# Kernel tuning notes

Measured on AMD Instinct MI355X. Metric: run time of the kernel, lower is better.

## Reference

```python
import jax, jax.numpy as jnp
import numpy as np

B, BINS, EMBED, HID, IND = 1, 500, 1024, 512, 128
POOL, MC_CROP, HIC_CROP = 5, 50, 10


def setup_inputs() -> dict:
    key = jax.random.key(0)
    ks = jax.random.split(key, 10)
    def w(k, shape, fan_in):
        return (jax.random.normal(k, shape, jnp.float32) / np.sqrt(fan_in)).astype(jnp.float32)
    return dict(
        x=jax.random.normal(ks[0], (B, BINS, EMBED), jnp.float32),
        # project MLP
        p_w1=w(ks[1], (EMBED, HID), EMBED), p_b1=jnp.zeros((HID,), jnp.float32),
        p_w2=w(ks[2], (HID, HID), HID), p_b2=jnp.zeros((HID,), jnp.float32),
        # pairattn_cop stub: per-pair linears (micro at full res, hic after 5x5 avg-pool)
        micro_w=w(ks[3], (HID, IND), HID), micro_b=jnp.zeros((IND,), jnp.float32),
        hic_w=w(ks[4], (HID, IND), HID), hic_b=jnp.zeros((IND,), jnp.float32),
        # prediction heads
        head_mc_w=w(ks[5], (IND, 2), IND), head_mc_b=jnp.zeros((2,), jnp.float32),
        head_ih_w1=w(ks[6], (IND, IND // 2), IND), head_ih_b1=jnp.zeros((IND // 2,), jnp.float32),
        head_ih_w2=w(ks[7], (IND // 2, 2), IND // 2), head_ih_b2=jnp.zeros((2,), jnp.float32),
        head_hic_w=w(ks[8], (IND, 3), IND), head_hic_b=jnp.zeros((3,), jnp.float32),
    )


def reference(x, p_w1, p_b1, p_w2, p_b2, micro_w, micro_b, hic_w, hic_b,
              head_mc_w, head_mc_b, head_ih_w1, head_ih_b1, head_ih_w2, head_ih_b2,
              head_hic_w, head_hic_b):
    # project: Linear -> ReLU -> Linear
    h = jax.nn.relu(x @ p_w1 + p_b1) @ p_w2 + p_b2            # [B, bins, HID]
    # output_head: fused pairwise outer-sum mean + scaled elementwise dot
    xi = h[:, :, None, :]                                      # [B, bins, 1, HID]
    xj = h[:, None, :, :]                                      # [B, 1, bins, HID]
    pair = (xi + xj) * 0.5 + xi * xj * (1.0 / np.sqrt(HID))    # [B, bins, bins, HID]
    # pairattn_cop stub
    micro = pair @ micro_w + micro_b                           # [B, bins, bins, IND]
    nb = BINS // POOL
    hic_in = pair.reshape(B, nb, POOL, nb, POOL, HID).mean(axis=(2, 4))  # [B, nb, nb, HID]
    hic = hic_in @ hic_w + hic_b                               # [B, nb, nb, IND]
    # prediction heads with crops
    mc = micro[:, MC_CROP:-MC_CROP, MC_CROP:-MC_CROP, :]       # [B, 400, 400, IND]
    out_mc = mc @ head_mc_w + head_mc_b
    out_ih = jax.nn.relu(mc @ head_ih_w1 + head_ih_b1) @ head_ih_w2 + head_ih_b2
    hc = hic[:, HIC_CROP:-HIC_CROP, HIC_CROP:-HIC_CROP, :]     # [B, 80, 80, IND]
    out_hic = hc @ head_hic_w + head_hic_b
    return (out_mc, out_ih, micro, out_hic)
```

## Files before the change

### kernel.cpp

```cpp
#include <hip/hip_runtime.h>

#define BINS 500
#define HID  512
#define INDD 128
#define PAIR_S 0.044194173824159216f

#define OFF_MC    0
#define OFF_IH    320000
#define OFF_MICRO 640000
#define OFF_HIC   32640000

#define WS_U     0
#define WS_MWT   64000
#define WS_HBF   96768
#define WS_H     256000
#define WS_HBAR  512000
#define WS_HWT   563200
#define WS_W1CT  595968

typedef __bf16 bf16;
typedef bf16 bf16x4 __attribute__((ext_vector_type(4)));
typedef bf16 bf16x8 __attribute__((ext_vector_type(8)));
typedef float f32x4 __attribute__((ext_vector_type(4)));

__device__ __forceinline__ bf16x8 join8(bf16x4 lo, bf16x4 hi) {
  return __builtin_shufflevector(lo, hi, 0, 1, 2, 3, 4, 5, 6, 7);
}
__device__ __forceinline__ bf16x4 cvt4(float a, float b, float c, float d) {
  bf16x4 r; r[0] = (bf16)a; r[1] = (bf16)b; r[2] = (bf16)c; r[3] = (bf16)d; return r;
}

__global__ void zero_init(float* __restrict__ ws) {
  int idx = (blockIdx.x * 256 + threadIdx.x) * 4;
  float4 z = {0.f, 0.f, 0.f, 0.f};
  *(float4*)(ws + idx) = z;
  *(float4*)(ws + WS_H + idx) = z;
}

__global__ __launch_bounds__(256, 2)
void gemm_ks(const float* __restrict__ A, const float* __restrict__ B,
             const float* __restrict__ abias, float* __restrict__ C,
             int M, int N, int K_per, int a_relu, float scale) {
  __shared__ float a_lds[64][36];
  __shared__ float bt_lds[64][36];
  const int t = threadIdx.x;
  const int w = t >> 6, l = t & 63;
  const int lr = l & 15, g = l >> 4;
  const int r0 = blockIdx.x * 64, n0 = blockIdx.y * 64;
  const int kbase = blockIdx.z * K_per;
  f32x4 acc[4] = {};
  for (int kq = 0; kq < K_per; kq += 32) {
    const int k0 = kbase + kq;
    {
      int row = t >> 2, kc = (t & 3) * 8;
      int gr = r0 + row; gr = gr < M ? gr : M - 1;
      const float* src = A + (size_t)gr * K_per * gridDim.z + k0 + kc;
      float4 v0 = *(const float4*)src;
      float4 v1 = *(const float4*)(src + 4);
      if (abias) {
        const float* bp = abias + k0 + kc;
        v0.x += bp[0]; v0.y += bp[1]; v0.z += bp[2]; v0.w += bp[3];
        v1.x += bp[4]; v1.y += bp[5]; v1.z += bp[6]; v1.w += bp[7];
        if (a_relu) {
          v0.x = fmaxf(v0.x, 0.f); v0.y = fmaxf(v0.y, 0.f);
          v0.z = fmaxf(v0.z, 0.f); v0.w = fmaxf(v0.w, 0.f);
          v1.x = fmaxf(v1.x, 0.f); v1.y = fmaxf(v1.y, 0.f);
          v1.z = fmaxf(v1.z, 0.f); v1.w = fmaxf(v1.w, 0.f);
        }
      }
      *(float4*)&a_lds[row][kc]     = v0;
      *(float4*)&a_lds[row][kc + 4] = v1;
    }
    {
      int n = t & 63, ks = (t >> 6) * 8;
      const float* src = B + (size_t)(k0 + ks) * N + n0 + n;
      #pragma unroll
      for (int s = 0; s < 8; s++) bt_lds[n][ks + s] = src[(size_t)s * N];
    }
    __syncthreads();
    bf16x8 ahi, alo;
    {
      int row = w * 16 + lr;
      float4 u0 = *(const float4*)&a_lds[row][g * 8];
      float4 u1 = *(const float4*)&a_lds[row][g * 8 + 4];
      float v[8] = {u0.x, u0.y, u0.z, u0.w, u1.x, u1.y, u1.z, u1.w};
      #pragma unroll
      for (int e = 0; e < 8; e++) {
        bf16 h = (bf16)v[e];
        ahi[e] = h; alo[e] = (bf16)(v[e] - (float)h);
      }
    }
    #pragma unroll
    for (int fn = 0; fn < 4; fn++) {
      int col = fn * 16 + lr;
      float4 u0 = *(const float4*)&bt_lds[col][g * 8];
      float4 u1 = *(const float4*)&bt_lds[col][g * 8 + 4];
      float v[8] = {u0.x, u0.y, u0.z, u0.w, u1.x, u1.y, u1.z, u1.w};
      bf16x8 bhi, blo;
      #pragma unroll
      for (int e = 0; e < 8; e++) {
        bf16 h = (bf16)v[e];
        bhi[e] = h; blo[e] = (bf16)(v[e] - (float)h);
      }
      acc[fn] = __builtin_amdgcn_mfma_f32_16x16x32_bf16(ahi, bhi, acc[fn], 0, 0, 0);
      acc[fn] = __builtin_amdgcn_mfma_f32_16x16x32_bf16(ahi, blo, acc[fn], 0, 0, 0);
      acc[fn] = __builtin_amdgcn_mfma_f32_16x16x32_bf16(alo, bhi, acc[fn], 0, 0, 0);
    }
    __syncthreads();
  }
  #pragma unroll
  for (int fn = 0; fn < 4; fn++) {
    int col = n0 + fn * 16 + lr;
    #pragma unroll
    for (int r = 0; r < 4; r++) {
      int row = r0 + w * 16 + g * 4 + r;
      if (row < M) atomicAdd(&C[(size_t)row * N + col], acc[fn][r] * scale);
    }
  }
}

__global__ void post_h(const float* __restrict__ h, const float* __restrict__ b2,
                       const float* __restrict__ micro_w,
                       const float* __restrict__ hic_w, const float* __restrict__ w_ih1,
                       const float* __restrict__ w_mc, float* __restrict__ ws) {
  int g = blockIdx.x * 256 + threadIdx.x;
  if (g < 256000) {
    bf16* hbf = (bf16*)(ws + WS_HBF);
    int k = g & (HID - 1);
    hbf[g] = (bf16)(h[g] + b2[k]);
  } else if (g < 256000 + 65536) {
    int gg = g - 256000;
    int n = gg >> 9, k = gg & 511;
    bf16* mwt = (bf16*)(ws + WS_MWT);
    mwt[gg] = (bf16)(PAIR_S * micro_w[k * INDD + n]);
  } else if (g < 256000 + 65536 + 51200) {
    int gg = g - (256000 + 65536);
    int a = gg >> 9, k = gg & (HID - 1);
    const float* p = h + (size_t)(a * 5) * HID + k;
    ws[WS_HBAR + gg] = 0.2f * (p[0] + p[HID] + p[2 * HID] + p[3 * HID] + p[4 * HID]) + b2[k];
  } else if (g < 256000 + 65536 + 51200 + 65536) {
    int gg = g - (256000 + 65536 + 51200);
    int n = gg >> 9, k = gg & 511;
    bf16* hwt = (bf16*)(ws + WS_HWT);
    hwt[gg] = (bf16)hic_w[k * INDD + n];
  } else if (g < 256000 + 65536 + 51200 + 65536 + 10240) {
    int gg = g - (256000 + 65536 + 51200 + 65536);
    int n = gg >> 7, k = gg & 127;
    float v = 0.f;
    if (n < 64) v = w_ih1[k * 64 + n];
    else if (n < 66) v = w_mc[k * 2 + (n - 64)];
    bf16* w1c = (bf16*)(ws + WS_W1CT);
    w1c[gg] = (bf16)v;
  } else if (g < 256000 + 65536 + 51200 + 65536 + 10240 + 64000) {
    int gg = g - (256000 + 65536 + 51200 + 65536 + 10240);
    ws[WS_U + gg] = 0.f;
  }
}

__global__ __launch_bounds__(256, 3)
void fused_micro_heads(const float* __restrict__ wsf, const float* __restrict__ micro_b,
                       const float* __restrict__ b1, const float* __restrict__ w2,
                       const float* __restrict__ bmc, const float* __restrict__ b2,
                       float* __restrict__ out) {
  __shared__ bf16 smem[16384];
  const int t = threadIdx.x;
  const int wv = t >> 6, l = t & 63;
  const int wj = wv >> 1, wn = wv & 1;
  const int lr = l & 15, g = l >> 4;
  const int i  = blockIdx.x;
  const int j0 = blockIdx.y * 128;
  const bf16* Hbf = (const bf16*)(wsf + WS_HBF);
  const bf16* mwt = (const bf16*)(wsf + WS_MWT);
  const float* U  = wsf + WS_U;
  const int bn = t >> 1, bh = t & 1;
  const int arow   = l >> 2;
  const int achunk = (l & 3) ^ ((l >> 3) & 3);
  const bf16* hbi = Hbf + (size_t)i * HID;
  f32x4 acc[4][4] = {};

  #pragma unroll
  for (int q = 0; q < 2; q++) {
    int row = wv * 32 + q * 16 + arow;
    int jj = j0 + row; jj = jj < BINS ? jj : BINS - 1;
    __builtin_amdgcn_global_load_lds(
        (const __attribute__((address_space(1))) void*)(Hbf + (size_t)jj * HID + achunk * 8),
        (__attribute__((address_space(3))) void*)(smem + (wv * 32 + q * 16) * 32),
        16, 0, 0);
  }
  {
    bf16x8 w0 = *(const bf16x8*)(mwt + (size_t)bn * HID + bh * 16);
    bf16x8 w1 = *(const bf16x8*)(mwt + (size_t)bn * HID + bh * 16 + 8);
    bf16x8 h0 = *(const bf16x8*)(hbi + bh * 16);
    bf16x8 h1 = *(const bf16x8*)(hbi + bh * 16 + 8);
    bf16x8 o0, o1;
    #pragma unroll
    for (int e = 0; e < 8; e++) o0[e] = (bf16)((float)h0[e] * (float)w0[e]);
    #pragma unroll
    for (int e = 0; e < 8; e++) o1[e] = (bf16)((float)h1[e] * (float)w1[e]);
    const int sw = (bn >> 1) & 3;
    *(bf16x8*)(smem + 8192 + bn * 32 + ((bh * 2)     ^ sw) * 8) = o0;
    *(bf16x8*)(smem + 8192 + bn * 32 + ((bh * 2 + 1) ^ sw) * 8) = o1;
  }
  asm volatile("s_waitcnt vmcnt(0) lgkmcnt(0)" ::: "memory");
  __builtin_amdgcn_s_barrier();

  int cur = 0;
  for (int kt = 0; kt < 16; kt++) {
    const bf16* htc = smem + cur * 4096;
    const bf16* btc = smem + 8192 + cur * 4096;
    bf16x8 w0, w1, h0, h1;
    if (kt < 15) {
      const int kn = (kt + 1) * 32;
      w0 = *(const bf16x8*)(mwt + (size_t)bn * HID + kn + bh * 16);
      w1 = *(const bf16x8*)(mwt + (size_t)bn * HID + kn + bh * 16 + 8);
      h0 = *(const bf16x8*)(hbi + kn + bh * 16);
      h1 = *(const bf16x8*)(hbi + kn + bh * 16 + 8);
      #pragma unroll
      for (int q = 0; q < 2; q++) {
        int row = wv * 32 + q * 16 + arow;
        int jj = j0 + row; jj = jj < BINS ? jj : BINS - 1;
        __builtin_amdgcn_global_load_lds(
            (const __attribute__((address_space(1))) void*)(Hbf + (size_t)jj * HID + kn + achunk * 8),
            (__attribute__((address_space(3))) void*)(smem + (cur ^ 1) * 4096 + (wv * 32 + q * 16) * 32),
            16, 0, 0);
      }
      asm volatile("s_waitcnt vmcnt(6)" ::: "memory");
    } else {
      asm volatile("s_waitcnt vmcnt(0)" ::: "memory");
    }
    bf16x8 af[4], bfr[4];
    const int s = g ^ ((lr >> 1) & 3);
    #pragma unroll
    for (int fm = 0; fm < 4; fm++)
      af[fm] = *(const bf16x8*)(htc + (wj * 64 + fm * 16 + lr) * 32 + s * 8);
    #pragma unroll
    for (int fn = 0; fn < 4; fn++)
      bfr[fn] = *(const bf16x8*)(btc + (wn * 64 + fn * 16 + lr) * 32 + s * 8);
    #pragma unroll
    for (int fm = 0; fm < 4; fm++)
      #pragma unroll
      for (int fn = 0; fn < 4; fn++)
        acc[fm][fn] = __builtin_amdgcn_mfma_f32_16x16x32_bf16(af[fm], bfr[fn], acc[fm][fn], 0, 0, 0);
    if (kt < 15) {
      bf16x8 o0, o1;
      #pragma unroll
      for (int e = 0; e < 8; e++) o0[e] = (bf16)((float)h0[e] * (float)w0[e]);
      #pragma unroll
      for (int e = 0; e < 8; e++) o1[e] = (bf16)((float)h1[e] * (float)w1[e]);
      bf16* btn = smem + 8192 + (cur ^ 1) * 4096;
      const int sw = (bn >> 1) & 3;
      *(bf16x8*)(btn + bn * 32 + ((bh * 2)     ^ sw) * 8) = o0;
      *(bf16x8*)(btn + bn * 32 + ((bh * 2 + 1) ^ sw) * 8) = o1;
    }
    asm volatile("s_waitcnt lgkmcnt(0)" ::: "memory");
    __builtin_amdgcn_s_barrier();
    cur ^= 1;
  }

  float Ui[4];
  #pragma unroll
  for (int fn = 0; fn < 4; fn++) {
    int n = wn * 64 + fn * 16 + lr;
    Ui[fn] = U[(size_t)i * INDD + n] + micro_b[n];
  }
  #pragma unroll
  for (int fm = 0; fm < 4; fm++) {
    #pragma unroll
    for (int r = 0; r < 4; r++) {
      int j = j0 + wj * 64 + fm * 16 + g * 4 + r;
      if (j < BINS) {
        const float* Uj = U + (size_t)j * INDD;
        size_t base = (size_t)OFF_MICRO + ((size_t)i * BINS + j) * INDD;
        #pragma unroll
        for (int fn = 0; fn < 4; fn++) {
          int n = wn * 64 + fn * 16 + lr;
          out[base + n] = acc[fm][fn][r] + Ui[fn] + Uj[n];
        }
      }
    }
  }
  asm volatile("s_waitcnt vmcnt(0)" ::: "memory");
  __builtin_amdgcn_s_barrier();

  if (i >= 50 && i < 450) {
    const bf16* w1c = (const bf16*)(wsf + WS_W1CT);
    f32x4 acc2[2][5] = {};
    const int jg = wv * 32;
    #pragma unroll
    for (int kt2 = 0; kt2 < 4; kt2++) {
      const int k0 = kt2 * 32;
      bf16x8 bfr[5];
      #pragma unroll
      for (int fn = 0; fn < 5; fn++) {
        int q = fn * 16 + lr;
        bfr[fn] = *(const bf16x8*)(w1c + q * 128 + k0 + g * 8);
      }
      bf16x8 af2[2];
      #pragma unroll
      for (int s16 = 0; s16 < 2; s16++) {
        int j = j0 + jg + s16 * 16 + lr;
        int jc = j < BINS ? j : BINS - 1;
        const float* src = out + (size_t)OFF_MICRO + ((size_t)i * BINS + jc) * INDD + k0 + g * 8;
        float4 v0 = *(const float4*)src;
        float4 v1 = *(const float4*)(src + 4);
        af2[s16] = join8(cvt4(v0.x, v0.y, v0.z, v0.w), cvt4(v1.x, v1.y, v1.z, v1.w));
      }
      #pragma unroll
      for (int s16 = 0; s16 < 2; s16++)
        #pragma unroll
        for (int fn = 0; fn < 5; fn++)
          acc2[s16][fn] = __builtin_amdgcn_mfma_f32_16x16x32_bf16(af2[s16], bfr[fn], acc2[s16][fn], 0, 0, 0);
    }
    float w2a[4], w2b[4], b1v[4];
    #pragma unroll
    for (int fn = 0; fn < 4; fn++) {
      int q = fn * 16 + lr;
      w2a[fn] = w2[q * 2]; w2b[fn] = w2[q * 2 + 1]; b1v[fn] = b1[q];
    }
    float bm = (lr < 2) ? bmc[lr] : 0.f;
    float b2a = b2[0], b2bv = b2[1];
    #pragma unroll
    for (int s16 = 0; s16 < 2; s16++) {
      #pragma unroll
      for (int r = 0; r < 4; r++) {
        int j = j0 + jg + s16 * 16 + g * 4 + r;
        float s0 = 0.f, s1 = 0.f;
        #pragma unroll
        for (int fn = 0; fn < 4; fn++) {
          float v = fmaxf(acc2[s16][fn][r] + b1v[fn], 0.f);
          s0 += v * w2a[fn]; s1 += v * w2b[fn];
        }
        #pragma unroll
        for (int mk = 1; mk < 16; mk <<= 1) {
          s0 += __shfl_xor(s0, mk);
          s1 += __shfl_xor(s1, mk);
        }
        if (j >= 50 && j < 450) {
          size_t mo = (size_t)(i - 50) * 400 + (j - 50);
          if (lr == 0) {
            out[OFF_IH + mo * 2]     = s0 + b2a;
            out[OFF_IH + mo * 2 + 1] = s1 + b2bv;
          }
          if (lr < 2) out[OFF_MC + mo * 2 + lr] = acc2[s16][4][r] + bm;
        }
      }
    }
  }
}

__device__ __forceinline__ bf16x4 pair4(float4 a, float4 b) {
  bf16x4 r;
  r[0] = (bf16)((a.x + b.x) * 0.5f + a.x * b.x * PAIR_S);
  r[1] = (bf16)((a.y + b.y) * 0.5f + a.y * b.y * PAIR_S);
  r[2] = (bf16)((a.z + b.z) * 0.5f + a.z * b.z * PAIR_S);
  r[3] = (bf16)((a.w + b.w) * 0.5f + a.w * b.w * PAIR_S);
  return r;
}

__global__ __launch_bounds__(256, 2)
void hic_kernel(const float* __restrict__ hbar, const float* __restrict__ wsf,
                const float* __restrict__ hicb, const float* __restrict__ whic,
                const float* __restrict__ bhic, float* __restrict__ out) {
  __shared__ float ha_lds[16][36];
  __shared__ float hb_lds[16][36];
  __shared__ bf16 pair_lds[256][36];
  __shared__ bf16 bt_lds[128][36];
  const int t = threadIdx.x;
  const int wv = t >> 6, l = t & 63;
  const int lr = l & 15, g = l >> 4;
  const int a0 = 10 + blockIdx.x * 16, b0 = 10 + blockIdx.y * 16;
  const bf16* hwt = (const bf16*)(wsf + WS_HWT);
  f32x4 acc[4][8] = {};
  for (int kt = 0; kt < 16; kt++) {
    const int k0 = kt * 32;
    if (t < 64) {
      int row = t >> 2, c = (t & 3) * 8;
      const float* src = hbar + (size_t)(a0 + row) * HID + k0 + c;
      *(float4*)&ha_lds[row][c]     = *(const float4*)src;
      *(float4*)&ha_lds[row][c + 4] = *(const float4*)(src + 4);
    } else if (t < 128) {
      int tt = t - 64;
      int row = tt >> 2, c = (tt & 3) * 8;
      const float* src = hbar + (size_t)(b0 + row) * HID + k0 + c;
      *(float4*)&hb_lds[row][c]     = *(const float4*)src;
      *(float4*)&hb_lds[row][c + 4] = *(const float4*)(src + 4);
    } else {
      int tt = t - 128;
      #pragma unroll
      for (int rep = 0; rep < 4; rep++) {
        int chunk = tt * 4 + rep;
        int n = chunk >> 2, part = chunk & 3;
        bf16x8 v = *(const bf16x8*)(hwt + (size_t)n * HID + k0 + part * 8);
        *(bf16x4*)&bt_lds[n][part * 8]     = __builtin_shufflevector(v, v, 0, 1, 2, 3);
        *(bf16x4*)&bt_lds[n][part * 8 + 4] = __builtin_shufflevector(v, v, 4, 5, 6, 7);
      }
    }
    __syncthreads();
    {
      int m = t;
      const float* pa = &ha_lds[m >> 4][0];
      const float* pb = &hb_lds[m & 15][0];
      #pragma unroll
      for (int c = 0; c < 4; c++) {
        float4 av0 = *(const float4*)(pa + c * 8);
        float4 av1 = *(const float4*)(pa + c * 8 + 4);
        float4 bv0 = *(const float4*)(pb + c * 8);
        float4 bv1 = *(const float4*)(pb + c * 8 + 4);
        *(bf16x4*)&pair_lds[m][c * 8]     = pair4(av0, bv0);
        *(bf16x4*)&pair_lds[m][c * 8 + 4] = pair4(av1, bv1);
      }
    }
    __syncthreads();
    bf16x8 af[4], bfr[8];
    #pragma unroll
    for (int fm = 0; fm < 4; fm++) {
      int row = wv * 64 + fm * 16 + lr;
      af[fm] = join8(*(const bf16x4*)&pair_lds[row][g * 8],
                     *(const bf16x4*)&pair_lds[row][g * 8 + 4]);
    }
    #pragma unroll
    for (int fn = 0; fn < 8; fn++) {
      int col = fn * 16 + lr;
      bfr[fn] = join8(*(const bf16x4*)&bt_lds[col][g * 8],
                      *(const bf16x4*)&bt_lds[col][g * 8 + 4]);
    }
    #pragma unroll
    for (int fm = 0; fm < 4; fm++)
      #pragma unroll
      for (int fn = 0; fn < 8; fn++)
        acc[fm][fn] = __builtin_amdgcn_mfma_f32_16x16x32_bf16(af[fm], bfr[fn], acc[fm][fn], 0, 0, 0);
    __syncthreads();
  }
  float wh0[8], wh1[8], wh2[8], hbv[8];
  #pragma unroll
  for (int fn = 0; fn < 8; fn++) {
    int n = fn * 16 + lr;
    wh0[fn] = whic[n * 3]; wh1[fn] = whic[n * 3 + 1]; wh2[fn] = whic[n * 3 + 2];
    hbv[fn] = hicb[n];
  }
  float bh0 = bhic[0], bh1 = bhic[1], bh2 = bhic[2];
  #pragma unroll
  for (int fm = 0; fm < 4; fm++) {
    #pragma unroll
    for (int r = 0; r < 4; r++) {
      int m = wv * 64 + fm * 16 + g * 4 + r;
      float s0 = 0.f, s1 = 0.f, s2 = 0.f;
      #pragma unroll
      for (int fn = 0; fn < 8; fn++) {
        float v = acc[fm][fn][r] + hbv[fn];
        s0 += v * wh0[fn]; s1 += v * wh1[fn]; s2 += v * wh2[fn];
      }
      #pragma unroll
      for (int mk = 1; mk < 16; mk <<= 1) {
        s0 += __shfl_xor(s0, mk);
        s1 += __shfl_xor(s1, mk);
        s2 += __shfl_xor(s2, mk);
      }
      if (lr == 0) {
        int aa = a0 + (m >> 4) - 10, bb = b0 + (m & 15) - 10;
        size_t o = (size_t)OFF_HIC + (size_t)(aa * 80 + bb) * 3;
        out[o] = s0 + bh0; out[o + 1] = s1 + bh1; out[o + 2] = s2 + bh2;
      }
    }
  }
}

extern "C" void kernel_launch(void* const* d_in, const int* in_sizes, int n_in,
                              void* d_out, int out_size, void* d_ws, size_t ws_size,
                              hipStream_t stream) {
  (void)in_sizes; (void)n_in; (void)out_size; (void)ws_size;
  const float* x    = (const float*)d_in[0];
  const float* pw1  = (const float*)d_in[1];
  const float* pb1  = (const float*)d_in[2];
  const float* pw2  = (const float*)d_in[3];
  const float* pb2  = (const float*)d_in[4];
  const float* mw   = (const float*)d_in[5];
  const float* mb   = (const float*)d_in[6];
  const float* hw   = (const float*)d_in[7];
  const float* hb   = (const float*)d_in[8];
  const float* wmc  = (const float*)d_in[9];
  const float* bmc  = (const float*)d_in[10];
  const float* wih1 = (const float*)d_in[11];
  const float* bih1 = (const float*)d_in[12];
  const float* wih2 = (const float*)d_in[13];
  const float* bih2 = (const float*)d_in[14];
  const float* whic = (const float*)d_in[15];
  const float* bhic = (const float*)d_in[16];
  float* out = (float*)d_out;
  float* ws  = (float*)d_ws;

  zero_init<<<250, 256, 0, stream>>>(ws);
  gemm_ks<<<dim3(8, 8, 4), 256, 0, stream>>>(x, pw1, nullptr, ws, 500, 512, 256, 0, 1.f);
  gemm_ks<<<dim3(8, 8, 2), 256, 0, stream>>>(ws, pw2, pb1, ws + WS_H, 500, 512, 256, 1, 1.f);
  post_h<<<2252, 256, 0, stream>>>(ws + WS_H, pb2, mw, hw, wih1, wmc, ws);
  gemm_ks<<<dim3(8, 2, 4), 256, 0, stream>>>(ws + WS_H, mw, pb2, ws + WS_U, 500, 128, 128, 0, 0.5f);
  fused_micro_heads<<<dim3(500, 4), 256, 0, stream>>>(ws, mb, bih1, wih2, bmc, bih2, out);
  hic_kernel<<<dim3(5, 5), 256, 0, stream>>>(ws + WS_HBAR, ws, hb, whic, bhic, out);
}
```

Before: 172.7 us.

## Split micro GEMM and prediction heads into separate kernels

Removes the heads epilogue from the fused micro kernel and runs it in a new heads_direct kernel over the 160000 cropped positions, reading micro back from global memory. The micro kernel gets lighter, with higher occupancy (launch bounds 3 to 4), and no block sits idle on the crop-boundary rows. In exchange it adds a kernel launch and re-reads the cropped micro tensor (about 80 MB in fp32), which may or may not still be cache-resident.

```diff
diff --git a/kernel.cpp b/kernel.cpp
--- a/kernel.cpp
+++ b/kernel.cpp
@@ -157,12 +157,11 @@
   }
 }
 
-__global__ __launch_bounds__(256, 3)
-void fused_micro_heads(const float* __restrict__ wsf, const float* __restrict__ micro_b,
-                       const float* __restrict__ b1, const float* __restrict__ w2,
-                       const float* __restrict__ bmc, const float* __restrict__ b2,
-                       float* __restrict__ out) {
-  __shared__ bf16 smem[16384];
+__global__ __launch_bounds__(256, 4)
+void fused_micro(const float* __restrict__ wsf, const float* __restrict__ micro_b,
+                 float* __restrict__ out) {
+  __shared__ bf16 Ht[2][128 * 32];
+  __shared__ bf16 Bt[2][128 * 32];
   const int t = threadIdx.x;
   const int wv = t >> 6, l = t & 63;
   const int wj = wv >> 1, wn = wv & 1;
@@ -184,7 +183,7 @@
     int jj = j0 + row; jj = jj < BINS ? jj : BINS - 1;
     __builtin_amdgcn_global_load_lds(
         (const __attribute__((address_space(1))) void*)(Hbf + (size_t)jj * HID + achunk * 8),
-        (__attribute__((address_space(3))) void*)(smem + (wv * 32 + q * 16) * 32),
+        (__attribute__((address_space(3))) void*)(&Ht[0][(wv * 32 + q * 16) * 32]),
         16, 0, 0);
   }
   {
@@ -198,16 +197,16 @@
     #pragma unroll
     for (int e = 0; e < 8; e++) o1[e] = (bf16)((float)h1[e] * (float)w1[e]);
     const int sw = (bn >> 1) & 3;
-    *(bf16x8*)(smem + 8192 + bn * 32 + ((bh * 2)     ^ sw) * 8) = o0;
-    *(bf16x8*)(smem + 8192 + bn * 32 + ((bh * 2 + 1) ^ sw) * 8) = o1;
+    *(bf16x8*)(&Bt[0][0] + bn * 32 + ((bh * 2)     ^ sw) * 8) = o0;
+    *(bf16x8*)(&Bt[0][0] + bn * 32 + ((bh * 2 + 1) ^ sw) * 8) = o1;
   }
   asm volatile("s_waitcnt vmcnt(0) lgkmcnt(0)" ::: "memory");
   __builtin_amdgcn_s_barrier();
 
   int cur = 0;
   for (int kt = 0; kt < 16; kt++) {
-    const bf16* htc = smem + cur * 4096;
-    const bf16* btc = smem + 8192 + cur * 4096;
+    const bf16* htc = &Ht[cur][0];
+    const bf16* btc = &Bt[cur][0];
     bf16x8 w0, w1, h0, h1;
     if (kt < 15) {
       const int kn = (kt + 1) * 32;
@@ -221,7 +220,7 @@
         int jj = j0 + row; jj = jj < BINS ? jj : BINS - 1;
         __builtin_amdgcn_global_load_lds(
             (const __attribute__((address_space(1))) void*)(Hbf + (size_t)jj * HID + kn + achunk * 8),
-            (__attribute__((address_space(3))) void*)(smem + (cur ^ 1) * 4096 + (wv * 32 + q * 16) * 32),
+            (__attribute__((address_space(3))) void*)(&Ht[cur ^ 1][(wv * 32 + q * 16) * 32]),
             16, 0, 0);
       }
       asm volatile("s_waitcnt vmcnt(6)" ::: "memory");
@@ -247,7 +246,7 @@
       for (int e = 0; e < 8; e++) o0[e] = (bf16)((float)h0[e] * (float)w0[e]);
       #pragma unroll
       for (int e = 0; e < 8; e++) o1[e] = (bf16)((float)h1[e] * (float)w1[e]);
-      bf16* btn = smem + 8192 + (cur ^ 1) * 4096;
+      bf16* btn = &Bt[cur ^ 1][0];
       const int sw = (bn >> 1) & 3;
       *(bf16x8*)(btn + bn * 32 + ((bh * 2)     ^ sw) * 8) = o0;
       *(bf16x8*)(btn + bn * 32 + ((bh * 2 + 1) ^ sw) * 8) = o1;
@@ -279,71 +278,75 @@
       }
     }
   }
-  asm volatile("s_waitcnt vmcnt(0)" ::: "memory");
-  __builtin_amdgcn_s_barrier();
-
-  if (i >= 50 && i < 450) {
-    const bf16* w1c = (const bf16*)(wsf + WS_W1CT);
-    f32x4 acc2[2][5] = {};
-    const int jg = wv * 32;
-    #pragma unroll
-    for (int kt2 = 0; kt2 < 4; kt2++) {
-      const int k0 = kt2 * 32;
-      bf16x8 bfr[5];
-      #pragma unroll
-      for (int fn = 0; fn < 5; fn++) {
-        int q = fn * 16 + lr;
-        bfr[fn] = *(const bf16x8*)(w1c + q * 128 + k0 + g * 8);
-      }
-      bf16x8 af2[2];
-      #pragma unroll
-      for (int s16 = 0; s16 < 2; s16++) {
-        int j = j0 + jg + s16 * 16 + lr;
-        int jc = j < BINS ? j : BINS - 1;
-        const float* src = out + (size_t)OFF_MICRO + ((size_t)i * BINS + jc) * INDD + k0 + g * 8;
-        float4 v0 = *(const float4*)src;
-        float4 v1 = *(const float4*)(src + 4);
-        af2[s16] = join8(cvt4(v0.x, v0.y, v0.z, v0.w), cvt4(v1.x, v1.y, v1.z, v1.w));
-      }
-      #pragma unroll
-      for (int s16 = 0; s16 < 2; s16++)
-        #pragma unroll
-        for (int fn = 0; fn < 5; fn++)
-          acc2[s16][fn] = __builtin_amdgcn_mfma_f32_16x16x32_bf16(af2[s16], bfr[fn], acc2[s16][fn], 0, 0, 0);
-    }
-    float w2a[4], w2b[4], b1v[4];
-    #pragma unroll
-    for (int fn = 0; fn < 4; fn++) {
+}
+
+__global__ __launch_bounds__(256, 2)
+void heads_direct(const float* __restrict__ micro, const float* __restrict__ wsf,
+                  const float* __restrict__ b1, const float* __restrict__ w2,
+                  const float* __restrict__ bmc, const float* __restrict__ b2,
+                  float* __restrict__ out) {
+  const int t = threadIdx.x;
+  const int wv = t >> 6, l = t & 63;
+  const int lr = l & 15, g = l >> 4;
+  const int mm0 = blockIdx.x * 256;
+  const bf16* w1c = (const bf16*)(wsf + WS_W1CT);
+  int mrow[4];
+  #pragma unroll
+  for (int fm = 0; fm < 4; fm++) {
+    int mm = mm0 + wv * 64 + fm * 16 + lr;
+    mrow[fm] = 25050 + mm + 100 * (mm / 400);
+  }
+  f32x4 acc[4][5] = {};
+  #pragma unroll
+  for (int kt = 0; kt < 4; kt++) {
+    const int k0 = kt * 32;
+    bf16x8 bfr[5];
+    #pragma unroll
+    for (int fn = 0; fn < 5; fn++) {
       int q = fn * 16 + lr;
-      w2a[fn] = w2[q * 2]; w2b[fn] = w2[q * 2 + 1]; b1v[fn] = b1[q];
-    }
-    float bm = (lr < 2) ? bmc[lr] : 0.f;
-    float b2a = b2[0], b2bv = b2[1];
-    #pragma unroll
-    for (int s16 = 0; s16 < 2; s16++) {
-      #pragma unroll
-      for (int r = 0; r < 4; r++) {
-        int j = j0 + jg + s16 * 16 + g * 4 + r;
-        float s0 = 0.f, s1 = 0.f;
-        #pragma unroll
-        for (int fn = 0; fn < 4; fn++) {
-          float v = fmaxf(acc2[s16][fn][r] + b1v[fn], 0.f);
-          s0 += v * w2a[fn]; s1 += v * w2b[fn];
-        }
-        #pragma unroll
-        for (int mk = 1; mk < 16; mk <<= 1) {
-          s0 += __shfl_xor(s0, mk);
-          s1 += __shfl_xor(s1, mk);
-        }
-        if (j >= 50 && j < 450) {
-          size_t mo = (size_t)(i - 50) * 400 + (j - 50);
-          if (lr == 0) {
-            out[OFF_IH + mo * 2]     = s0 + b2a;
-            out[OFF_IH + mo * 2 + 1] = s1 + b2bv;
-          }
-          if (lr < 2) out[OFF_MC + mo * 2 + lr] = acc2[s16][4][r] + bm;
-        }
-      }
+      bfr[fn] = *(const bf16x8*)(w1c + q * 128 + k0 + g * 8);
+    }
+    #pragma unroll
+    for (int fm = 0; fm < 4; fm++) {
+      const float* src = micro + (size_t)mrow[fm] * INDD + k0 + g * 8;
+      float4 v0 = *(const float4*)src;
+      float4 v1 = *(const float4*)(src + 4);
+      bf16x8 af = join8(cvt4(v0.x, v0.y, v0.z, v0.w), cvt4(v1.x, v1.y, v1.z, v1.w));
+      #pragma unroll
+      for (int fn = 0; fn < 5; fn++)
+        acc[fm][fn] = __builtin_amdgcn_mfma_f32_16x16x32_bf16(af, bfr[fn], acc[fm][fn], 0, 0, 0);
+    }
+  }
+  float w2a[4], w2b[4], b1v[4];
+  #pragma unroll
+  for (int fn = 0; fn < 4; fn++) {
+    int q = fn * 16 + lr;
+    w2a[fn] = w2[q * 2]; w2b[fn] = w2[q * 2 + 1]; b1v[fn] = b1[q];
+  }
+  float bm = (lr < 2) ? bmc[lr] : 0.f;
+  float b2a = b2[0], b2bv = b2[1];
+  #pragma unroll
+  for (int fm = 0; fm < 4; fm++) {
+    #pragma unroll
+    for (int r = 0; r < 4; r++) {
+      int m = wv * 64 + fm * 16 + g * 4 + r;
+      float s0 = 0.f, s1 = 0.f;
+      #pragma unroll
+      for (int fn = 0; fn < 4; fn++) {
+        float v = fmaxf(acc[fm][fn][r] + b1v[fn], 0.f);
+        s0 += v * w2a[fn]; s1 += v * w2b[fn];
+      }
+      #pragma unroll
+      for (int mk = 1; mk < 16; mk <<= 1) {
+        s0 += __shfl_xor(s0, mk);
+        s1 += __shfl_xor(s1, mk);
+      }
+      size_t mo = (size_t)(mm0 + m);
+      if (lr == 0) {
+        out[OFF_IH + mo * 2]     = s0 + b2a;
+        out[OFF_IH + mo * 2 + 1] = s1 + b2bv;
+      }
+      if (lr < 2) out[OFF_MC + mo * 2 + lr] = acc[fm][4][r] + bm;
     }
   }
 }
@@ -494,6 +497,7 @@
   gemm_ks<<<dim3(8, 8, 2), 256, 0, stream>>>(ws, pw2, pb1, ws + WS_H, 500, 512, 256, 1, 1.f);
   post_h<<<2252, 256, 0, stream>>>(ws + WS_H, pb2, mw, hw, wih1, wmc, ws);
   gemm_ks<<<dim3(8, 2, 4), 256, 0, stream>>>(ws + WS_H, mw, pb2, ws + WS_U, 500, 128, 128, 0, 0.5f);
-  fused_micro_heads<<<dim3(500, 4), 256, 0, stream>>>(ws, mb, bih1, wih2, bmc, bih2, out);
+  fused_micro<<<dim3(500, 4), 256, 0, stream>>>(ws, mb, out);
+  heads_direct<<<625, 256, 0, stream>>>(out + OFF_MICRO, ws, bih1, wih2, bmc, bih2, out);
   hic_kernel<<<dim3(5, 5), 256, 0, stream>>>(ws + WS_HBAR, ws, hb, whic, bhic, out);
 }
```

Measured after the change: 167.3 us. 3.2% less time.
